# Performance work log

Hardware: AMD Instinct MI355X
Metric: run time of the kernel (lower is better)

Reference implementation:

```python
import jax, jax.numpy as jnp
import numpy as np

NORM_EPS = 1e-05

def _quant_input(x):
    # per-token dynamic int8 fake-quant: s = 127 / max(|x|, 1e-5)
    s = 127.0 / jnp.clip(jnp.max(jnp.abs(x), axis=-1, keepdims=True), 1e-05, None)
    return jnp.clip(jnp.round(x * s), -128.0, 127.0) / s

def _rmsnorm(x, w, eps):
    return x * jax.lax.rsqrt(jnp.mean(x * x, axis=-1, keepdims=True) + eps) * w

def setup_inputs() -> dict:
    key = jax.random.key(0)
    k0, k1, k2 = jax.random.split(key, 3)
    dim, hidden = 2048, 5632
    x = jax.random.normal(k0, (4, 2048, dim), dtype=jnp.float32)
    w13 = jax.random.normal(k1, (2 * hidden, dim), dtype=jnp.float32) * 0.02
    w2 = jax.random.normal(k2, (dim, hidden), dtype=jnp.float32) * 0.02
    norm_w = jnp.ones((hidden,), dtype=jnp.float32)
    return {"x": x, "w13": w13, "w2": w2, "norm_w": norm_w}

def reference(x, w13, w2, norm_w):
    # BitLinear w13: quantize input, then linear
    xq = _quant_input(x)
    x13 = jnp.einsum('bsd,fd->bsf', xq, w13)  # [B,S,2H]
    x1, x3 = jnp.split(x13, 2, axis=-1)
    gated = jnp.square(jax.nn.relu(x1)) * x3  # squared-ReLU gating
    inner = _rmsnorm(gated, norm_w, NORM_EPS)
    # BitLinear w2
    iq = _quant_input(inner)
    out = jnp.einsum('bsh,dh->bsd', iq, w2)
    return out
```

## Files before the change

kernel.cpp:

```cpp
#include <hip/hip_runtime.h>

typedef unsigned short u16;
typedef __attribute__((ext_vector_type(8))) short short8;
typedef __attribute__((ext_vector_type(4))) float f32x4;
typedef __attribute__((ext_vector_type(4))) u16 ushort4v;
typedef __attribute__((ext_vector_type(8))) u16 ushort8v;

#define DIM 2048
#define HID 5632
#define F2  11264
#define TTOT 8192

#define GLD(g, l) __builtin_amdgcn_global_load_lds(                       \
    (const __attribute__((address_space(1))) void*)(g),                   \
    (__attribute__((address_space(3))) void*)(l), 16, 0, 0)

__device__ __forceinline__ u16 f2bf(float f) {
  unsigned int u = __builtin_bit_cast(unsigned int, f);
  u += 0x7FFFu + ((u >> 16) & 1u);
  return (u16)(u >> 16);
}

__global__ __launch_bounds__(256) void conv_w13(const float* __restrict__ w,
                                                u16* __restrict__ o) {
  int idx = blockIdx.x * 256 + threadIdx.x;
  int rnew = idx >> 9;
  int dc = (idx & 511) << 2;
  int b = rnew >> 5, ii = rnew & 31;
  int orig = (ii < 16) ? (b * 16 + ii) : (HID + b * 16 + (ii - 16));
  float4 v = *reinterpret_cast<const float4*>(w + (size_t)orig * DIM + dc);
  ushort4v q = {f2bf(v.x), f2bf(v.y), f2bf(v.z), f2bf(v.w)};
  *reinterpret_cast<ushort4v*>(o + (size_t)rnew * DIM + dc) = q;
}

__global__ __launch_bounds__(256) void conv_w2(const float* __restrict__ w,
                                               u16* __restrict__ o) {
  size_t e = ((size_t)blockIdx.x * 256 + threadIdx.x) * 4;
  float4 v = *reinterpret_cast<const float4*>(w + e);
  ushort4v q = {f2bf(v.x), f2bf(v.y), f2bf(v.z), f2bf(v.w)};
  *reinterpret_cast<ushort4v*>(o + e) = q;
}

__global__ __launch_bounds__(256) void quant_x(const float* __restrict__ x,
                                               u16* __restrict__ q,
                                               float* __restrict__ scale) {
  const int t = blockIdx.x;
  const float* xr = x + (size_t)t * DIM;
  const int tid = threadIdx.x;
  float4 a = *reinterpret_cast<const float4*>(xr + tid * 8);
  float4 b = *reinterpret_cast<const float4*>(xr + tid * 8 + 4);
  float v[8] = {a.x, a.y, a.z, a.w, b.x, b.y, b.z, b.w};
  float m = 0.f;
#pragma unroll
  for (int i = 0; i < 8; ++i) m = fmaxf(m, fabsf(v[i]));
#pragma unroll
  for (int off = 32; off; off >>= 1) m = fmaxf(m, __shfl_xor(m, off));
  __shared__ float red[4];
  if ((tid & 63) == 0) red[tid >> 6] = m;
  __syncthreads();
  m = fmaxf(fmaxf(red[0], red[1]), fmaxf(red[2], red[3]));
  m = fmaxf(m, 1e-5f);
  float s = 127.0f / m;
  if (tid == 0) scale[t] = m / 127.0f;
  ushort8v o;
#pragma unroll
  for (int i = 0; i < 8; ++i) {
    float r = fminf(fmaxf(rintf(v[i] * s), -128.f), 127.f);
    o[i] = f2bf(r);
  }
  *reinterpret_cast<ushort8v*>(q + (size_t)t * DIM + tid * 8) = o;
}

__global__ __launch_bounds__(256) void gate_nq(const float* __restrict__ G,
                                               const float* __restrict__ nw,
                                               u16* __restrict__ q2,
                                               float* __restrict__ s2) {
  const int t = blockIdx.x;
  const float* gr = G + (size_t)t * HID;
  const int tid = threadIdx.x;
  float4 vv[6];
  float ss = 0.f, mx = 0.f;
#pragma unroll
  for (int k = 0; k < 6; ++k) {
    int i = tid + k * 256;
    if (i < 1408) {
      float4 v = *reinterpret_cast<const float4*>(gr + i * 4);
      float4 w4 = *reinterpret_cast<const float4*>(nw + i * 4);
      vv[k] = v;
      ss += v.x * v.x + v.y * v.y + v.z * v.z + v.w * v.w;
      mx = fmaxf(mx, fmaxf(fmaxf(fabsf(v.x * w4.x), fabsf(v.y * w4.y)),
                           fmaxf(fabsf(v.z * w4.z), fabsf(v.w * w4.w))));
    }
  }
#pragma unroll
  for (int off = 32; off; off >>= 1) {
    ss += __shfl_xor(ss, off);
    mx = fmaxf(mx, __shfl_xor(mx, off));
  }
  __shared__ float rs[4], rm[4];
  if ((tid & 63) == 0) { rs[tid >> 6] = ss; rm[tid >> 6] = mx; }
  __syncthreads();
  ss = rs[0] + rs[1] + rs[2] + rs[3];
  mx = fmaxf(fmaxf(rm[0], rm[1]), fmaxf(rm[2], rm[3]));
  float rinv = 1.0f / sqrtf(ss * (1.0f / 5632.0f) + 1e-5f);
  float mi = fmaxf(mx * rinv, 1e-5f);
  float s = 127.0f / mi;
  if (tid == 0) s2[t] = mi / 127.0f;
  float fs = rinv * s;
#pragma unroll
  for (int k = 0; k < 6; ++k) {
    int i = tid + k * 256;
    if (i < 1408) {
      float4 v = vv[k];
      float4 w4 = *reinterpret_cast<const float4*>(nw + i * 4);
      ushort4v o;
      o.x = f2bf(fminf(fmaxf(rintf(v.x * w4.x * fs), -128.f), 127.f));
      o.y = f2bf(fminf(fmaxf(rintf(v.y * w4.y * fs), -128.f), 127.f));
      o.z = f2bf(fminf(fmaxf(rintf(v.z * w4.z * fs), -128.f), 127.f));
      o.w = f2bf(fminf(fmaxf(rintf(v.w * w4.w * fs), -128.f), 127.f));
      *reinterpret_cast<ushort4v*>(q2 + (size_t)t * HID + i * 4) = o;
    }
  }
}

template <int GATE, int N, int K, int Ntiles>
__global__ __launch_bounds__(512, 2) void gemm8(
    const u16* __restrict__ A, const u16* __restrict__ B,
    const float* __restrict__ rowscale, float* __restrict__ C) {
  __shared__ __attribute__((aligned(16))) u16 lds[2][2][2][256 * 32];
  constexpr int NT = K >> 6;
  const int nwg = gridDim.x;
  const int orig = blockIdx.x;
  const int qq = nwg >> 3, rr = nwg & 7, xcd = orig & 7, sidx = orig >> 3;
  const int wg = (xcd < rr ? xcd * (qq + 1) : rr * (qq + 1) + (xcd - rr) * qq) + sidx;
  const int mt = wg / Ntiles, nt = wg % Ntiles;

  const int tid = threadIdx.x;
  const int wid = tid >> 6, lane = tid & 63;
  const int wm = wid >> 2, wn = wid & 3;
  const int c16 = lane & 15, q4 = lane >> 4;
  const int rA_base = wm * 128 + c16;
  const int rB_base = wn * 64 + c16;
  const int caf = (q4 ^ ((lane >> 1) & 3)) << 3;

  const int sr = tid >> 2;
  const int scol = ((tid & 3) ^ ((tid >> 3) & 3)) << 3;
  const u16* Ar = A + ((size_t)mt * 256 + sr) * K + scol;
  const u16* Br = B + ((size_t)nt * 256 + sr) * K + scol;
  constexpr size_t rstep = (size_t)128 * K;

  f32x4 acc[8][4];
#pragma unroll
  for (int m = 0; m < 8; ++m)
#pragma unroll
    for (int n = 0; n < 4; ++n) acc[m][n] = f32x4{0.f, 0.f, 0.f, 0.f};

#define STAGE(MAT, KK, T, BUF)                                                \
  {                                                                           \
    const u16* g = ((MAT) ? Br : Ar) + (T) * 64 + (KK) * 32;                  \
    u16* l = &lds[BUF][MAT][KK][wid << 9];                                    \
    GLD(g, l);                                                                \
    GLD(g + rstep, l + 4096);                                                 \
  }
#define LDA(DB, KK, MH, AF)                                                   \
  _Pragma("unroll") for (int m = 0; m < 4; ++m)                               \
      AF[m] = *reinterpret_cast<const short8*>(                               \
          &lds[DB][0][KK][(rA_base + ((MH) * 4 + m) * 16) * 32 + caf]);
#define LDB(DB, KK, BF)                                                       \
  _Pragma("unroll") for (int n = 0; n < 4; ++n)                               \
      BF[n] = *reinterpret_cast<const short8*>(                               \
          &lds[DB][1][KK][(rB_base + n * 16) * 32 + caf]);
#define MFMA32(AF0, AF1, BF)                                                  \
  __builtin_amdgcn_s_setprio(1);                                              \
  _Pragma("unroll") for (int m = 0; m < 4; ++m)                               \
      _Pragma("unroll") for (int n = 0; n < 4; ++n)                           \
          acc[m][n] = __builtin_amdgcn_mfma_f32_16x16x32_bf16(                \
              AF0[m], BF[n], acc[m][n], 0, 0, 0);                             \
  _Pragma("unroll") for (int m = 0; m < 4; ++m)                               \
      _Pragma("unroll") for (int n = 0; n < 4; ++n)                           \
          acc[4 + m][n] = __builtin_amdgcn_mfma_f32_16x16x32_bf16(            \
              AF1[m], BF[n], acc[4 + m][n], 0, 0, 0);                         \
  __builtin_amdgcn_s_setprio(0);                                              \
  __builtin_amdgcn_sched_barrier(0);
#define BARR asm volatile("s_barrier" ::: "memory")
#define VMC(NN) asm volatile("s_waitcnt vmcnt(" #NN ")" ::: "memory")

#define KT2(DB, U, STGA, VMA, STGB, VMB)                                      \
  {                                                                           \
    short8 bfr[4], af0[4], af1[4];                                            \
                                                            \
    LDB(DB, 0, bfr)                                                           \
    LDA(DB, 0, 0, af0)                                                        \
    LDA(DB, 0, 1, af1)                                                        \
    if (STGA) {                                                               \
      STAGE(0, 1, (U) + 1, (DB) ^ 1)                                          \
      STAGE(1, 1, (U) + 1, (DB) ^ 1)                                          \
    }                                                                         \
    MFMA32(af0, af1, bfr)                                                     \
    VMC(VMA);                                                                 \
    BARR;                                                                     \
                                                            \
    LDB(DB, 1, bfr)                                                           \
    LDA(DB, 1, 0, af0)                                                        \
    LDA(DB, 1, 1, af1)                                                        \
    if (STGB) {                                                               \
      STAGE(0, 0, (U) + 2, DB)                                                \
      STAGE(1, 0, (U) + 2, DB)                                                \
    }                                                                         \
    MFMA32(af0, af1, bfr)                                                     \
    VMC(VMB);                                                                 \
    BARR;                                                                     \
  }

  STAGE(1, 0, 0, 0) STAGE(0, 0, 0, 0) STAGE(1, 1, 0, 0) STAGE(0, 1, 0, 0)
  STAGE(1, 0, 1, 1) STAGE(0, 0, 1, 1)
  VMC(4);
  BARR;

#pragma unroll 1
  for (int u = 0; u < NT - 2; u += 2) {
    KT2(0, u, 1, 8, 1, 8)
    KT2(1, u + 1, 1, 8, 1, 8)
  }
  KT2(0, NT - 2, 1, 8, 0, 8)
  KT2(1, NT - 1, 0, 0, 0, 0)

  const int mbase0 = mt * 256 + wm * 128;
  if constexpr (GATE == 0) {
#pragma unroll
    for (int m = 0; m < 8; ++m) {
#pragma unroll
      for (int j = 0; j < 4; ++j) {
        const int row = mbase0 + m * 16 + q4 * 4 + j;
        const float sc = rowscale[row];
        float* crow = C + (size_t)row * N + nt * 256 + wn * 64 + c16;
#pragma unroll
        for (int n = 0; n < 4; ++n) crow[n * 16] = acc[m][n][j] * sc;
      }
    }
  } else {
    constexpr int H = N >> 1;
    const int gbase = (nt * 256 + wn * 64) >> 1;
#pragma unroll
    for (int m = 0; m < 8; ++m) {
#pragma unroll
      for (int j = 0; j < 4; ++j) {
        const int row = mbase0 + m * 16 + q4 * 4 + j;
        const float sc = rowscale[row];
        const float s3 = sc * sc * sc;
        float* grow = C + (size_t)row * H + gbase + c16;
#pragma unroll
        for (int p = 0; p < 2; ++p) {
          float a1 = acc[m][2 * p][j];
          float a3 = acc[m][2 * p + 1][j];
          float rl = fmaxf(a1, 0.f);
          grow[p * 16] = rl * rl * a3 * s3;
        }
      }
    }
  }
}

extern "C" void kernel_launch(void* const* d_in, const int* in_sizes, int n_in,
                              void* d_out, int out_size, void* d_ws, size_t ws_size,
                              hipStream_t stream) {
  const float* x = (const float*)d_in[0];
  const float* w13 = (const float*)d_in[1];
  const float* w2 = (const float*)d_in[2];
  const float* nw = (const float*)d_in[3];
  float* out = (float*)d_out;

  char* p = (char*)d_ws;
  u16* w13p = (u16*)p; p += (size_t)F2 * DIM * 2;
  u16* w2b = (u16*)p;  p += (size_t)DIM * HID * 2;
  u16* q2f = (u16*)p;  p += (size_t)TTOT * HID * 2;
  float* s2f = (float*)p; p += (size_t)TTOT * 4;
  const size_t fixed = (size_t)F2 * DIM * 2 + (size_t)DIM * HID * 2 +
                       (size_t)TTOT * HID * 2 + (size_t)TTOT * 4;
  const size_t perTok = (size_t)DIM * 2 + (size_t)HID * 4 + 8;
  int Tc = TTOT;
  while (Tc > 256 && fixed + (size_t)Tc * perTok > ws_size) Tc >>= 1;
  u16* q1 = (u16*)p;        p += (size_t)Tc * DIM * 2;
  float* gated = (float*)p; p += (size_t)Tc * HID * 4;
  float* s1 = (float*)p;

  conv_w13<<<F2 * DIM / 4 / 256, 256, 0, stream>>>(w13, w13p);
  conv_w2<<<DIM * HID / 4 / 256, 256, 0, stream>>>(w2, w2b);

  for (int t0 = 0; t0 < TTOT; t0 += Tc) {
    quant_x<<<Tc, 256, 0, stream>>>(x + (size_t)t0 * DIM, q1, s1);
    gemm8<1, F2, DIM, F2 / 256><<<(Tc / 256) * (F2 / 256), 512, 0, stream>>>(
        q1, w13p, s1, gated);
    gate_nq<<<Tc, 256, 0, stream>>>(gated, nw, q2f + (size_t)t0 * HID, s2f + t0);
  }
  gemm8<0, DIM, HID, DIM / 256><<<(TTOT / 256) * (DIM / 256), 512, 0, stream>>>(
      q2f, w2b, s2f, out);
}
```

Baseline: 604.3 us.

## Software-pipeline LDS fragment loads one phase ahead of MFMA compute

Restructures the GEMM main loop to double-buffer register fragments, so the LDS reads for the next K half-tile are issued before the MFMAs on the current fragments. An explicit lgkmcnt wait keeps the MFMAs ordered after their own loads. The goal is to hide LDS read latency behind matrix math instead of stalling on each load. In exchange it needs twice as many fragment registers, which may lower occupancy, and the staging and vmcnt schedule has to be retuned.

After: 808.7 us. 33.8% more time.

```diff
diff --git a/kernel.cpp b/kernel.cpp
--- a/kernel.cpp
+++ b/kernel.cpp
@@ -184,31 +184,18 @@
   __builtin_amdgcn_sched_barrier(0);
 #define BARR asm volatile("s_barrier" ::: "memory")
 #define VMC(NN) asm volatile("s_waitcnt vmcnt(" #NN ")" ::: "memory")
-
-#define KT2(DB, U, STGA, VMA, STGB, VMB)                                      \
+#define LGKM12 do { asm volatile("s_waitcnt lgkmcnt(12)" ::: "memory");       \
+                    __builtin_amdgcn_sched_barrier(0); } while (0)
+
+#define PH(NDB, NKK, RB, RA0, RA1, CA0, CA1, CB, DOSTG, STKK, STT, STBUF, VM) \
   {                                                                           \
-    short8 bfr[4], af0[4], af1[4];                                            \
-                                                            \
-    LDB(DB, 0, bfr)                                                           \
-    LDA(DB, 0, 0, af0)                                                        \
-    LDA(DB, 0, 1, af1)                                                        \
-    if (STGA) {                                                               \
-      STAGE(0, 1, (U) + 1, (DB) ^ 1)                                          \
-      STAGE(1, 1, (U) + 1, (DB) ^ 1)                                          \
-    }                                                                         \
-    MFMA32(af0, af1, bfr)                                                     \
-    VMC(VMA);                                                                 \
-    BARR;                                                                     \
-                                                            \
-    LDB(DB, 1, bfr)                                                           \
-    LDA(DB, 1, 0, af0)                                                        \
-    LDA(DB, 1, 1, af1)                                                        \
-    if (STGB) {                                                               \
-      STAGE(0, 0, (U) + 2, DB)                                                \
-      STAGE(1, 0, (U) + 2, DB)                                                \
-    }                                                                         \
-    MFMA32(af0, af1, bfr)                                                     \
-    VMC(VMB);                                                                 \
+    LDB(NDB, NKK, RB)                                                         \
+    LDA(NDB, NKK, 0, RA0)                                                     \
+    LDA(NDB, NKK, 1, RA1)                                                     \
+    if (DOSTG) { STAGE(0, STKK, STT, STBUF) STAGE(1, STKK, STT, STBUF) }      \
+    LGKM12;                                                                   \
+    MFMA32(CA0, CA1, CB)                                                      \
+    VM;                                                                       \
     BARR;                                                                     \
   }
 
@@ -217,13 +204,24 @@
   VMC(4);
   BARR;
 
+  short8 bA[4], a0A[4], a1A[4], bB[4], a0B[4], a1B[4];
+  LDB(0, 0, bA) LDA(0, 0, 0, a0A) LDA(0, 0, 1, a1A)
+
 #pragma unroll 1
   for (int u = 0; u < NT - 2; u += 2) {
-    KT2(0, u, 1, 8, 1, 8)
-    KT2(1, u + 1, 1, 8, 1, 8)
-  }
-  KT2(0, NT - 2, 1, 8, 0, 8)
-  KT2(1, NT - 1, 0, 0, 0, 0)
+    PH(0, 1, bB, a0B, a1B, a0A, a1A, bA, 1, 1, u + 1, 1, VMC(4))
+    PH(1, 0, bA, a0A, a1A, a0B, a1B, bB, 1, 0, u + 2, 0, VMC(4))
+    PH(1, 1, bB, a0B, a1B, a0A, a1A, bA, 1, 1, u + 2, 0, VMC(4))
+    PH(0, 0, bA, a0A, a1A, a0B, a1B, bB, 1, 0, u + 3, 1, VMC(4))
+  }
+  PH(0, 1, bB, a0B, a1B, a0A, a1A, bA, 1, 1, NT - 1, 1, VMC(4))
+  PH(1, 0, bA, a0A, a1A, a0B, a1B, bB, 0, 0, 0, 0, VMC(0))
+  LDB(1, 1, bB) LDA(1, 1, 0, a0B) LDA(1, 1, 1, a1B)
+  LGKM12;
+  MFMA32(a0A, a1A, bA)
+  asm volatile("s_waitcnt lgkmcnt(0)" ::: "memory");
+  __builtin_amdgcn_sched_barrier(0);
+  MFMA32(a0B, a1B, bB)
 
   const int mbase0 = mt * 256 + wm * 128;
   if constexpr (GATE == 0) {
```
